# Kernel tuning notes

Measured on AMD Instinct MI355X. Metric: run time of the kernel, lower is better.

## Reference

```python
import jax, jax.numpy as jnp
import numpy as np

N = 50000
IN_CH = 512
OUT_CH = 512
DEG = 32
E = N * DEG


def setup_inputs() -> dict:
    key = jax.random.key(0)
    kx, kwc, kwn, kb, ke = jax.random.split(key, 5)
    x = jax.random.normal(kx, (N, IN_CH), dtype=jnp.float32)
    bound = 1.0 / np.sqrt(IN_CH)
    wc = jax.random.uniform(kwc, (IN_CH, OUT_CH), minval=-bound, maxval=bound, dtype=jnp.float32)
    wn = jax.random.uniform(kwn, (IN_CH, OUT_CH), minval=-bound, maxval=bound, dtype=jnp.float32)
    bias = jax.random.uniform(kb, (OUT_CH,), minval=-bound, maxval=bound, dtype=jnp.float32)
    # Every node appears as a source exactly DEG times -> no empty-neighborhood NaNs.
    src = jnp.repeat(jnp.arange(N, dtype=jnp.int64), DEG)
    dst = jax.random.randint(ke, (E,), 0, N, dtype=jnp.int64)
    edge_index = jnp.stack([src, dst], axis=0)  # [2, E]
    return {"x": x, "wc": wc, "wn": wn, "bias": bias, "edge_index": edge_index}


def reference(x, wc, wn, bias, edge_index):
    # alpha = x @ wc ; beta = x @ wn
    alpha = x @ wc                       # [N, out]
    beta = x @ wn                        # [N, out]
    src, dst = edge_index[0], edge_index[1]
    # gamma[n] = mean_{e: src[e]==n} beta[dst[e]]
    sums = jax.ops.segment_sum(beta[dst], src, num_segments=x.shape[0])          # [N, out]
    counts = jax.ops.segment_sum(jnp.ones_like(src, dtype=beta.dtype), src,
                                 num_segments=x.shape[0])                        # [N]
    gamma = sums / counts[:, None]
    return alpha + gamma + bias
```

## Files before the change

kernel.cpp:

```cpp
#include <hip/hip_runtime.h>


#define M_ROWS 50000
#define DEG 32
#define NE (M_ROWS * DEG)
#define SLICE_DW 800000

typedef short s16x8 __attribute__((ext_vector_type(8)));
typedef float f32x4 __attribute__((ext_vector_type(4)));
typedef float f32x2 __attribute__((ext_vector_type(2)));
typedef unsigned int u32x2 __attribute__((ext_vector_type(2)));

__device__ __forceinline__ unsigned short f2bf(float f) {
  union { float f; unsigned int u; } c; c.f = f;
  unsigned int u = c.u;
  u += 0x7fffu + ((u >> 16) & 1u);
  return (unsigned short)(u >> 16);
}

__device__ __forceinline__ unsigned char f2fp8(float f) {
  int p = __builtin_amdgcn_cvt_pk_fp8_f32(f, f, 0, false);
  return (unsigned char)(p & 0xff);
}

__device__ __forceinline__ float bfhi(unsigned int u) {
  return __uint_as_float(u & 0xffff0000u);
}
__device__ __forceinline__ float bflo(unsigned int u) {
  return __uint_as_float(u << 16);
}

__device__ __forceinline__ void gl_lds16(const void* g, void* l) {
  __builtin_amdgcn_global_load_lds(
      (const __attribute__((address_space(1))) unsigned int*)g,
      (__attribute__((address_space(3))) unsigned int*)l, 16, 0, 0);
}

__global__ __launch_bounds__(256) void k_convert_x(
    const float* __restrict__ x, unsigned short* __restrict__ xb) {
  const size_t base = ((size_t)blockIdx.x * 256 + threadIdx.x) * 8;
  const float4 a = *(const float4*)(x + base);
  const float4 b = *(const float4*)(x + base + 4);
  union { unsigned short u[8]; uint4 v; } p;
  p.u[0] = f2bf(a.x); p.u[1] = f2bf(a.y); p.u[2] = f2bf(a.z); p.u[3] = f2bf(a.w);
  p.u[4] = f2bf(b.x); p.u[5] = f2bf(b.y); p.u[6] = f2bf(b.z); p.u[7] = f2bf(b.w);
  *(uint4*)(xb + base) = p.v;
}

__global__ __launch_bounds__(256) void k_convert_w(
    const float* __restrict__ wc, const float* __restrict__ wn,
    unsigned short* __restrict__ wt) {
  const int k = blockIdx.x;
  const int n4 = threadIdx.x * 4;
  const float* src = (n4 < 512) ? (wc + (size_t)k * 512 + n4)
                                : (wn + (size_t)k * 512 + (n4 - 512));
  const float4 v = *(const float4*)src;
  wt[(size_t)(n4 + 0) * 512 + k] = f2bf(v.x);
  wt[(size_t)(n4 + 1) * 512 + k] = f2bf(v.y);
  wt[(size_t)(n4 + 2) * 512 + k] = f2bf(v.z);
  wt[(size_t)(n4 + 3) * 512 + k] = f2bf(v.w);
}

__global__ __launch_bounds__(256) void k_gemm(
    const unsigned short* __restrict__ xb,
    const unsigned short* __restrict__ wt,
    const float* __restrict__ bias,
    unsigned short* __restrict__ alphab,
    unsigned char* __restrict__ betaf8) {
  __shared__ __attribute__((aligned(16))) unsigned short As[128 * 64];
  __shared__ __attribute__((aligned(16))) unsigned short Bs[128 * 64];

  const int tid = threadIdx.x;
  const int g = blockIdx.x;
  int mt, nt;
  if (g < 3072) {
    const int c = g & 7, j = g >> 3;
    nt = j & 7; mt = (j >> 3) * 8 + c;
  } else {
    const int r = g - 3072;
    mt = 384 + (r >> 3); nt = r & 7;
  }
  const int n0 = nt * 128;
  const int m0 = mt * 128;

  const int wv = tid >> 6;
  const int l = tid & 63;
  const int lm = l & 15;
  const int quad = l >> 4;
  const int mb = (wv >> 1) * 64;
  const int nb = (wv & 1) * 64;

  size_t aofs[4], bofs[4];
  int ldst[4];
#pragma unroll
  for (int s = 0; s < 4; ++s) {
    const int c = s * 256 + tid;
    const int row = c >> 3;
    const int seg = c & 7;
    const int sg = seg ^ (row & 7);
    int am = m0 + row; if (am >= M_ROWS) am = M_ROWS - 1;
    aofs[s] = (size_t)am * 512 + sg * 8;
    bofs[s] = (size_t)(n0 + row) * 512 + sg * 8;
    ldst[s] = (s * 256 + (tid & ~63)) * 16;
  }

  f32x4 acc[4][4];
#pragma unroll
  for (int i = 0; i < 4; ++i)
#pragma unroll
    for (int j = 0; j < 4; ++j) acc[i][j] = (f32x4)(0.0f);

  for (int kt = 0; kt < 8; ++kt) {
    const int k0 = kt * 64;
    __syncthreads();
#pragma unroll
    for (int s = 0; s < 4; ++s) {
      gl_lds16(xb + aofs[s] + k0, (char*)As + ldst[s]);
      gl_lds16(wt + bofs[s] + k0, (char*)Bs + ldst[s]);
    }
    __syncthreads();

#pragma unroll
    for (int h = 0; h < 2; ++h) {
      s16x8 af[4], bfr[4];
#pragma unroll
      for (int i = 0; i < 4; ++i) {
        const int R = mb + 16 * i + lm;
        af[i] = *(const s16x8*)&As[R * 64 + (((h * 4 + quad) ^ (R & 7)) << 3)];
      }
#pragma unroll
      for (int j = 0; j < 4; ++j) {
        const int R = nb + 16 * j + lm;
        bfr[j] = *(const s16x8*)&Bs[R * 64 + (((h * 4 + quad) ^ (R & 7)) << 3)];
      }
#pragma unroll
      for (int i = 0; i < 4; ++i)
#pragma unroll
        for (int j = 0; j < 4; ++j)
          acc[i][j] = __builtin_amdgcn_mfma_f32_16x16x32_bf16(
              af[i], bfr[j], acc[i][j], 0, 0, 0);
    }
  }

  const bool isAlpha = (n0 < 512);
  float b4[4];
#pragma unroll
  for (int j = 0; j < 4; ++j)
    b4[j] = isAlpha ? bias[n0 + nb + 16 * j + lm] : 0.0f;

#pragma unroll
  for (int i = 0; i < 4; ++i) {
#pragma unroll
    for (int j = 0; j < 4; ++j) {
#pragma unroll
      for (int r = 0; r < 4; ++r) {
        const int m = m0 + mb + 16 * i + quad * 4 + r;
        if (m < M_ROWS) {
          const int n = n0 + nb + 16 * j + lm;
          const float v = acc[i][j][r];
          if (isAlpha) {
            alphab[(size_t)m * 512 + n] = f2bf(v + b4[j]);
          } else {
            const int nc = n - 512;
            betaf8[(size_t)(nc >> 6) * (SLICE_DW * 4) + (size_t)m * 64 + (nc & 63)] =
                f2fp8(v);
          }
        }
      }
    }
  }
}

__global__ __launch_bounds__(256) void k_gather(
    const int* __restrict__ dst, const unsigned int* __restrict__ beta8,
    const unsigned short* __restrict__ alphab, float* __restrict__ out) {
  const int phase = blockIdx.y;
  const int node = blockIdx.x * 4 + (threadIdx.x >> 6);
  const int l = threadIdx.x & 63;
  const int grp = l >> 4;
  const int lm = l & 15;
  const int idx = __builtin_nontemporal_load(dst + (size_t)node * 32 + (l & 31));

  const unsigned int* bp = beta8 + (size_t)phase * SLICE_DW + lm;
  f32x2 s01 = (f32x2)(0.0f), s23 = (f32x2)(0.0f);
#pragma unroll
  for (int j = 0; j < 8; ++j) {
    const int row = __shfl(idx, j * 4 + grp, 64);
    const unsigned int b = bp[(size_t)row * 16];
    s01 += __builtin_amdgcn_cvt_pk_f32_fp8(b, false);
    s23 += __builtin_amdgcn_cvt_pk_f32_fp8(b, true);
  }
#pragma unroll
  for (int off = 16; off < 64; off <<= 1) {
    s01.x += __shfl_xor(s01.x, off, 64);
    s01.y += __shfl_xor(s01.y, off, 64);
    s23.x += __shfl_xor(s23.x, off, 64);
    s23.y += __shfl_xor(s23.y, off, 64);
  }
  if (l < 16) {
    const size_t o = (size_t)node * 512 + phase * 64 + lm * 4;
    const u32x2 av = __builtin_nontemporal_load(
        (const u32x2*)(alphab + o));
    const float s = 1.0f / 32.0f;
    f32x4 v;
    v.x = bflo(av.x) + s01.x * s;
    v.y = bfhi(av.x) + s01.y * s;
    v.z = bflo(av.y) + s23.x * s;
    v.w = bfhi(av.y) + s23.y * s;
    __builtin_nontemporal_store(v, (f32x4*)(out + o));
  }
}

extern "C" void kernel_launch(void* const* d_in, const int* in_sizes, int n_in,
                              void* d_out, int out_size, void* d_ws, size_t ws_size,
                              hipStream_t stream) {
  const float* x    = (const float*)d_in[0];
  const float* wc   = (const float*)d_in[1];
  const float* wn   = (const float*)d_in[2];
  const float* bias = (const float*)d_in[3];
  const int*   ei   = (const int*)d_in[4];
  float* out = (float*)d_out;

  char* ws = (char*)d_ws;
  unsigned short* xb     = (unsigned short*)ws;
  unsigned short* wt     = (unsigned short*)(ws + 51200000);
  unsigned short* alphab = (unsigned short*)(ws + 52248576);
  unsigned char*  betaf8 = (unsigned char*)(ws + 103448576);

  k_convert_x<<<12500, 256, 0, stream>>>(x, xb);
  k_convert_w<<<512, 256, 0, stream>>>(wc, wn, wt);
  k_gemm<<<3128, 256, 0, stream>>>(xb, wt, bias, alphab, betaf8);
  k_gather<<<dim3(12500, 8), 256, 0, stream>>>(ei + NE, (const unsigned int*)betaf8,
                                               alphab, out);
}
```

Measured before the change: 416.5 us.

## Pack GEMM epilogue stores, convert dst indices to u16, reorder gather grid

The GEMM epilogue now packs four columns per thread into one wider store, both bf16 alpha and fp8 beta, using a permuted column layout that the gather kernel reads back. Destination indices are narrowed to 16-bit in a new pre-kernel, halving index traffic in the gather. The gather grid is flattened so the 8 column phases of a node run in adjacent blocks, which should improve locality of alpha/out. Output stores become four scalar strided stores instead of one float4, and the u16 path depends on workspace size.

```diff
diff --git a/kernel.cpp b/kernel.cpp
--- a/kernel.cpp
+++ b/kernel.cpp
@@ -16,11 +16,6 @@
   unsigned int u = c.u;
   u += 0x7fffu + ((u >> 16) & 1u);
   return (unsigned short)(u >> 16);
-}
-
-__device__ __forceinline__ unsigned char f2fp8(float f) {
-  int p = __builtin_amdgcn_cvt_pk_fp8_f32(f, f, 0, false);
-  return (unsigned char)(p & 0xff);
 }
 
 __device__ __forceinline__ float bfhi(unsigned int u) {
@@ -61,6 +56,20 @@
   wt[(size_t)(n4 + 3) * 512 + k] = f2bf(v.w);
 }
 
+__global__ __launch_bounds__(256) void k_convert_dst(
+    const int* __restrict__ dst, unsigned short* __restrict__ d16) {
+  const size_t base = ((size_t)blockIdx.x * 256 + threadIdx.x) * 8;
+  if (base >= NE) return;
+  const int4 a = *(const int4*)(dst + base);
+  const int4 b = *(const int4*)(dst + base + 4);
+  union { unsigned short u[8]; uint4 v; } p;
+  p.u[0] = (unsigned short)a.x; p.u[1] = (unsigned short)a.y;
+  p.u[2] = (unsigned short)a.z; p.u[3] = (unsigned short)a.w;
+  p.u[4] = (unsigned short)b.x; p.u[5] = (unsigned short)b.y;
+  p.u[6] = (unsigned short)b.z; p.u[7] = (unsigned short)b.w;
+  *(uint4*)(d16 + base) = p.v;
+}
+
 __global__ __launch_bounds__(256) void k_gemm(
     const unsigned short* __restrict__ xb,
     const unsigned short* __restrict__ wt,
@@ -143,45 +152,59 @@
   }
 
   const bool isAlpha = (n0 < 512);
+  const int grp64 = (n0 + nb) >> 6;
   float b4[4];
 #pragma unroll
   for (int j = 0; j < 4; ++j)
     b4[j] = isAlpha ? bias[n0 + nb + 16 * j + lm] : 0.0f;
 
-#pragma unroll
-  for (int i = 0; i < 4; ++i) {
-#pragma unroll
-    for (int j = 0; j < 4; ++j) {
+  if (isAlpha) {
+    unsigned int* ap = (unsigned int*)alphab;
+#pragma unroll
+    for (int i = 0; i < 4; ++i) {
 #pragma unroll
       for (int r = 0; r < 4; ++r) {
         const int m = m0 + mb + 16 * i + quad * 4 + r;
         if (m < M_ROWS) {
-          const int n = n0 + nb + 16 * j + lm;
-          const float v = acc[i][j][r];
-          if (isAlpha) {
-            alphab[(size_t)m * 512 + n] = f2bf(v + b4[j]);
-          } else {
-            const int nc = n - 512;
-            betaf8[(size_t)(nc >> 6) * (SLICE_DW * 4) + (size_t)m * 64 + (nc & 63)] =
-                f2fp8(v);
-          }
+          u32x2 v;
+          v.x = (unsigned int)f2bf(acc[i][0][r] + b4[0]) |
+                ((unsigned int)f2bf(acc[i][1][r] + b4[1]) << 16);
+          v.y = (unsigned int)f2bf(acc[i][2][r] + b4[2]) |
+                ((unsigned int)f2bf(acc[i][3][r] + b4[3]) << 16);
+          *(u32x2*)(ap + (size_t)m * 256 + grp64 * 32 + 2 * lm) = v;
         }
       }
     }
-  }
-}
-
+  } else {
+    unsigned int* bp = (unsigned int*)betaf8 + (size_t)(grp64 - 8) * SLICE_DW;
+#pragma unroll
+    for (int i = 0; i < 4; ++i) {
+#pragma unroll
+      for (int r = 0; r < 4; ++r) {
+        const int m = m0 + mb + 16 * i + quad * 4 + r;
+        if (m < M_ROWS) {
+          int p = __builtin_amdgcn_cvt_pk_fp8_f32(acc[i][0][r], acc[i][1][r], 0, false);
+          p = __builtin_amdgcn_cvt_pk_fp8_f32(acc[i][2][r], acc[i][3][r], p, true);
+          bp[(size_t)m * 16 + lm] = (unsigned int)p;
+        }
+      }
+    }
+  }
+}
+
+template <typename IT>
 __global__ __launch_bounds__(256) void k_gather(
-    const int* __restrict__ dst, const unsigned int* __restrict__ beta8,
-    const unsigned short* __restrict__ alphab, float* __restrict__ out) {
-  const int phase = blockIdx.y;
-  const int node = blockIdx.x * 4 + (threadIdx.x >> 6);
+    const IT* __restrict__ dst, const unsigned int* __restrict__ beta32,
+    const unsigned int* __restrict__ alpha32, float* __restrict__ out) {
+  const int gb = blockIdx.x;
+  const int phase = gb & 7;
+  const int node = (gb >> 3) * 4 + (threadIdx.x >> 6);
   const int l = threadIdx.x & 63;
   const int grp = l >> 4;
   const int lm = l & 15;
-  const int idx = __builtin_nontemporal_load(dst + (size_t)node * 32 + (l & 31));
-
-  const unsigned int* bp = beta8 + (size_t)phase * SLICE_DW + lm;
+  const int idx = (int)__builtin_nontemporal_load(dst + (size_t)node * 32 + (l & 31));
+
+  const unsigned int* bp = beta32 + (size_t)phase * SLICE_DW + lm;
   f32x2 s01 = (f32x2)(0.0f), s23 = (f32x2)(0.0f);
 #pragma unroll
   for (int j = 0; j < 8; ++j) {
@@ -198,16 +221,14 @@
     s23.y += __shfl_xor(s23.y, off, 64);
   }
   if (l < 16) {
-    const size_t o = (size_t)node * 512 + phase * 64 + lm * 4;
     const u32x2 av = __builtin_nontemporal_load(
-        (const u32x2*)(alphab + o));
+        (const u32x2*)(alpha32 + (size_t)node * 256 + phase * 32) + lm);
     const float s = 1.0f / 32.0f;
-    f32x4 v;
-    v.x = bflo(av.x) + s01.x * s;
-    v.y = bfhi(av.x) + s01.y * s;
-    v.z = bflo(av.y) + s23.x * s;
-    v.w = bfhi(av.y) + s23.y * s;
-    __builtin_nontemporal_store(v, (f32x4*)(out + o));
+    float* ob = out + (size_t)node * 512 + phase * 64;
+    __builtin_nontemporal_store(bflo(av.x) + s01.x * s, ob + lm);
+    __builtin_nontemporal_store(bfhi(av.x) + s01.y * s, ob + 16 + lm);
+    __builtin_nontemporal_store(bflo(av.y) + s23.x * s, ob + 32 + lm);
+    __builtin_nontemporal_store(bfhi(av.y) + s23.y * s, ob + 48 + lm);
   }
 }
 
@@ -226,10 +247,18 @@
   unsigned short* wt     = (unsigned short*)(ws + 51200000);
   unsigned short* alphab = (unsigned short*)(ws + 52248576);
   unsigned char*  betaf8 = (unsigned char*)(ws + 103448576);
+  unsigned short* d16    = (unsigned short*)(ws + 129048576);
+  const bool u16ok = (ws_size >= (size_t)129048576 + 3200000);
 
   k_convert_x<<<12500, 256, 0, stream>>>(x, xb);
   k_convert_w<<<512, 256, 0, stream>>>(wc, wn, wt);
+  if (u16ok) k_convert_dst<<<782, 256, 0, stream>>>(ei + NE, d16);
   k_gemm<<<3128, 256, 0, stream>>>(xb, wt, bias, alphab, betaf8);
-  k_gather<<<dim3(12500, 8), 256, 0, stream>>>(ei + NE, (const unsigned int*)betaf8,
-                                               alphab, out);
-}
+  if (u16ok) {
+    k_gather<unsigned short><<<100000, 256, 0, stream>>>(
+        d16, (const unsigned int*)betaf8, (const unsigned int*)alphab, out);
+  } else {
+    k_gather<int><<<100000, 256, 0, stream>>>(
+        ei + NE, (const unsigned int*)betaf8, (const unsigned int*)alphab, out);
+  }
+}
```

New measurement: 385.8 us. 7.4% less time.
